# Kernel tuning notes

Measured on AMD Instinct MI355X. Metric: run time of the kernel, lower is better.

The kernel has to match this reference:

```python
import jax, jax.numpy as jnp
import numpy as np

N_NODES = 100000
N_EDGES = 1600000
FEAT = 128
HID = 128
CLASSES = 10
GRAPHS = 64


def gcn_conv(x, W, b, src, dst, n):
    # PyG GCNConv: h = x @ W; add self-loops; symmetric deg^{-1/2} norm; scatter-add; + bias
    h = x @ W
    src_f = jnp.concatenate([src, jnp.arange(n, dtype=src.dtype)])
    dst_f = jnp.concatenate([dst, jnp.arange(n, dtype=dst.dtype)])
    deg = jax.ops.segment_sum(jnp.ones_like(dst_f, dtype=h.dtype), dst_f, num_segments=n)
    dinv = jax.lax.rsqrt(jnp.where(deg > 0, deg, 1.0))
    norm = dinv[src_f] * dinv[dst_f]              # [E+N]
    msg = h[src_f] * norm[:, None]                # gather + scale
    out = jax.ops.segment_sum(msg, dst_f, num_segments=n)  # scatter-add
    return out + b


def global_mean_pool(x, batch, num_graphs):
    s = jax.ops.segment_sum(x, batch, num_segments=num_graphs)
    cnt = jax.ops.segment_sum(jnp.ones_like(batch, dtype=x.dtype), batch, num_segments=num_graphs)
    return s / jnp.maximum(cnt, 1.0)[:, None]


def setup_inputs() -> dict:
    key = jax.random.key(0)
    ks = jax.random.split(key, 10)
    x = jax.random.normal(ks[0], (N_NODES, FEAT), dtype=jnp.float32)
    edge_index = jax.random.randint(ks[1], (2, N_EDGES), 0, N_NODES, dtype=jnp.int64)
    batch = jnp.sort(jax.random.randint(ks[2], (N_NODES,), 0, GRAPHS, dtype=jnp.int64))
    def glorot(k, fi, fo):
        s = float(np.sqrt(6.0 / (fi + fo)))
        return jax.random.uniform(k, (fi, fo), jnp.float32, -s, s)
    return {
        "x": x, "edge_index": edge_index, "batch": batch,
        "W1": glorot(ks[3], FEAT, HID), "b1": jnp.zeros((HID,), jnp.float32),
        "W2": glorot(ks[4], HID, HID), "b2": jnp.zeros((HID,), jnp.float32),
        "W3": glorot(ks[5], HID, HID), "b3": jnp.zeros((HID,), jnp.float32),
        "Wlin": glorot(ks[6], HID, CLASSES), "blin": jnp.zeros((CLASSES,), jnp.float32),
    }


def reference(x, edge_index, batch, W1, b1, W2, b2, W3, b3, Wlin, blin):
    src, dst = edge_index[0], edge_index[1]
    n = x.shape[0]
    h = jax.nn.relu(gcn_conv(x, W1, b1, src, dst, n))
    h = jax.nn.relu(gcn_conv(h, W2, b2, src, dst, n))
    h = gcn_conv(h, W3, b3, src, dst, n)
    emb = global_mean_pool(h, batch, GRAPHS)      # [GRAPHS, HID]
    # dropout(p=0.5) is identity in eval mode
    logits = emb @ Wlin + blin                    # [GRAPHS, CLASSES]
    return logits, jnp.squeeze(emb)
```

## Files before the change

### kernel.cpp

```cpp
#include <hip/hip_runtime.h>
#include <hip/hip_bf16.h>
#include <stdint.h>

typedef unsigned int uint32;
typedef __attribute__((ext_vector_type(8))) short short8;
typedef __attribute__((ext_vector_type(4))) float float4v;
typedef __attribute__((ext_vector_type(2))) float f32x2;

#define FEAT 128
#define NGRAPH 64
#define GB   256
#define NBK  512
#define QPG  8

__device__ __forceinline__ float bf2f_lo(uint32 v) {
    union { uint32 i; float f; } u; u.i = v << 16; return u.f;
}
__device__ __forceinline__ float bf2f_hi(uint32 v) {
    union { uint32 i; float f; } u; u.i = v & 0xffff0000u; return u.f;
}
__device__ __forceinline__ unsigned short f2bf(float f) {
    uint32 u = __builtin_bit_cast(uint32, f);
    uint32 r = (u + 0x7fffu + ((u >> 16) & 1u)) >> 16;
    return (unsigned short)r;
}
__device__ __forceinline__ uint32 f2bf2(float lo, float hi) {
    return (uint32)f2bf(lo) | ((uint32)f2bf(hi) << 16);
}

__global__ void k_bhist(const int* __restrict__ dst, int* __restrict__ bhistT,
                        const float* __restrict__ W1, const float* __restrict__ W2,
                        const float* __restrict__ W3, unsigned short* __restrict__ o1,
                        unsigned short* __restrict__ o2, unsigned short* __restrict__ o3,
                        int E) {
    int t = threadIdx.x, blk = blockIdx.x;
    if (blk >= GB) {
        int b2 = blk - GB;
        int wid = b2 >> 3;
        const float* W = (wid == 0) ? W1 : (wid == 1) ? W2 : W3;
        unsigned short* out = (wid == 0) ? o1 : (wid == 1) ? o2 : o3;
        int e = (b2 & 7) * 256 + t;
        int kt = e >> 9, ct = (e >> 6) & 7, lane = e & 63;
        int krow = kt * 32 + (lane >> 4) * 8;
        int col = ct * 16 + (lane & 15);
#pragma unroll
        for (int j = 0; j < 8; j++)
            out[e * 8 + j] = f2bf(W[(krow + j) * FEAT + col]);
        return;
    }
    __shared__ int h[NBK];
    for (int b = t; b < NBK; b += 256) h[b] = 0;
    __syncthreads();
    int chunk = (E + GB - 1) / GB;
    int lo = blk * chunk, hi = min(lo + chunk, E);
    for (int e = lo + t; e < hi; e += 256)
        atomicAdd(&h[dst[e] >> 8], 1);
    __syncthreads();
    for (int b = t; b < NBK; b += 256) bhistT[b * GB + blk] = h[b];
}

__global__ void k_boffs_a(int* __restrict__ bhistT, int* __restrict__ btot) {
    int b = blockIdx.x, l = threadIdx.x;
    int v[4];
    int base = b * GB + l * 4;
#pragma unroll
    for (int j = 0; j < 4; j++) v[j] = bhistT[base + j];
    int s = v[0] + v[1] + v[2] + v[3];
    int incl = s;
    for (int off = 1; off < 64; off <<= 1) {
        int u = __shfl_up(incl, off);
        if (l >= off) incl += u;
    }
    int excl = incl - s;
    int p0 = excl, p1 = p0 + v[0], p2 = p1 + v[1], p3 = p2 + v[2];
    bhistT[base + 0] = p0; bhistT[base + 1] = p1;
    bhistT[base + 2] = p2; bhistT[base + 3] = p3;
    if (l == 63) btot[b] = incl;
}

__global__ void k_bscat(const int* __restrict__ src, const int* __restrict__ dst,
                        const int* __restrict__ bhistT, const int* __restrict__ btot,
                        uint32* __restrict__ ebuf, int E) {
    __shared__ int cur[NBK];
    int t = threadIdx.x, blk = blockIdx.x;
    int o0 = btot[t], o1 = btot[t + 256];
    cur[t] = o0; cur[t + 256] = o1;
    __syncthreads();
    for (int off = 1; off < NBK; off <<= 1) {
        int v0 = (t >= off) ? cur[t - off] : 0;
        int v1 = (t + 256 >= off) ? cur[t + 256 - off] : 0;
        __syncthreads();
        cur[t] += v0; cur[t + 256] += v1;
        __syncthreads();
    }
    cur[t]       = cur[t]       - o0 + bhistT[t * GB + blk];
    cur[t + 256] = cur[t + 256] - o1 + bhistT[(t + 256) * GB + blk];
    __syncthreads();
    int chunk = (E + GB - 1) / GB;
    int lo = blk * chunk, hi = min(lo + chunk, E);
    for (int e = lo + t; e < hi; e += 256) {
        int d = dst[e], s = src[e];
        int b = d >> 8;
        int p = atomicAdd(&cur[b], 1);
        ebuf[p] = ((uint32)s << 8) | (uint32)(d & 255);
    }
}

__global__ void k_csr(const uint32* __restrict__ ebuf, const int* __restrict__ btot,
                      float* __restrict__ dinv, int* __restrict__ rowp,
                      int* __restrict__ csrc, int N, int E) {
    __shared__ int h[256];
    __shared__ int cur[256];
    __shared__ int ebase;
    int t = threadIdx.x, b = blockIdx.x;
    int part = 0;
    for (int j = t; j < b; j += 256) part += btot[j];
    cur[t] = part;
    __syncthreads();
    for (int off = 128; off > 0; off >>= 1) {
        if (t < off) cur[t] += cur[t + off];
        __syncthreads();
    }
    if (t == 0) ebase = cur[0];
    __syncthreads();
    int e0 = ebase, e1 = e0 + btot[b];
    h[t] = 0;
    __syncthreads();
    for (int e = e0 + t; e < e1; e += 256)
        atomicAdd(&h[ebuf[e] & 255u], 1);
    __syncthreads();
    int deg = h[t];
    cur[t] = deg;
    __syncthreads();
    for (int off = 1; off < 256; off <<= 1) {
        int v = (t >= off) ? cur[t - off] : 0;
        __syncthreads();
        cur[t] += v;
        __syncthreads();
    }
    int r = e0 + cur[t] - deg;
    int node = b * 256 + t;
    if (node < N) {
        rowp[node] = r;
        dinv[node] = rsqrtf((float)deg + 1.0f);
    }
    if (b == 0 && t == 0) rowp[N] = E;
    cur[t] = r;
    __syncthreads();
    for (int e = e0 + t; e < e1; e += 256) {
        uint32 v = ebuf[e];
        int p = atomicAdd(&cur[v & 255u], 1);
        csrc[p] = (int)(v >> 8);
    }
}

template <bool F32IN>
__global__ void k_gemm(const void* __restrict__ Xp,
                       const unsigned short* __restrict__ Wswz,
                       const float* __restrict__ dinv,
                       unsigned short* __restrict__ Hb, int N, int ntiles) {
    __shared__ unsigned short Wl[FEAT * FEAT];
    {
        const uint4* Wg = (const uint4*)Wswz;
        uint4* Ws = (uint4*)Wl;
        for (int i = threadIdx.x; i < 2048; i += 256) Ws[i] = Wg[i];
    }
    __syncthreads();

    int wave = threadIdx.x >> 6, lane = threadIdx.x & 63;
    int m = lane & 15, q = lane >> 4;
    const short8* Bl = (const short8*)Wl;

    for (int tb = blockIdx.x; tb < ntiles; tb += gridDim.x) {
        int r0 = (tb * 4 + wave) * 16;
        if (r0 >= N) continue;

        int arow = r0 + m; if (arow >= N) arow = N - 1;
        short8 a[4];
        if (F32IN) {
            const float* Ar = (const float*)Xp + (long)arow * FEAT;
#pragma unroll
            for (int kt = 0; kt < 4; kt++) {
                float4 u = *(const float4*)(Ar + kt * 32 + q * 8);
                float4 v = *(const float4*)(Ar + kt * 32 + q * 8 + 4);
                short8 tv;
                tv[0] = (short)f2bf(u.x); tv[1] = (short)f2bf(u.y);
                tv[2] = (short)f2bf(u.z); tv[3] = (short)f2bf(u.w);
                tv[4] = (short)f2bf(v.x); tv[5] = (short)f2bf(v.y);
                tv[6] = (short)f2bf(v.z); tv[7] = (short)f2bf(v.w);
                a[kt] = tv;
            }
        } else {
            const short8* Ar = (const short8*)((const unsigned short*)Xp + (long)arow * FEAT);
#pragma unroll
            for (int kt = 0; kt < 4; kt++) a[kt] = Ar[kt * 4 + q];
        }

        float4v acc[8];
#pragma unroll
        for (int ct = 0; ct < 8; ct++) acc[ct] = (float4v){0.f, 0.f, 0.f, 0.f};
#pragma unroll
        for (int ct = 0; ct < 8; ct++) {
            acc[ct] = __builtin_amdgcn_mfma_f32_16x16x32_bf16(Bl[(0 * 8 + ct) * 64 + lane], a[0], acc[ct], 0, 0, 0);
            acc[ct] = __builtin_amdgcn_mfma_f32_16x16x32_bf16(Bl[(1 * 8 + ct) * 64 + lane], a[1], acc[ct], 0, 0, 0);
            acc[ct] = __builtin_amdgcn_mfma_f32_16x16x32_bf16(Bl[(2 * 8 + ct) * 64 + lane], a[2], acc[ct], 0, 0, 0);
            acc[ct] = __builtin_amdgcn_mfma_f32_16x16x32_bf16(Bl[(3 * 8 + ct) * 64 + lane], a[3], acc[ct], 0, 0, 0);
        }

        int node = r0 + m;
        bool ok = (node < N);
        float d = ok ? dinv[node] : 0.f;
#pragma unroll
        for (int ct = 0; ct < 8; ct++) {
            if (ok) {
                uint2 o;
                o.x = f2bf2(acc[ct][0] * d, acc[ct][1] * d);
                o.y = f2bf2(acc[ct][2] * d, acc[ct][3] * d);
                ((uint2*)(Hb + (long)node * FEAT + ct * 16))[q] = o;
            }
        }
    }
}

template <int RELU>
__global__ void k_agg(const uint32* __restrict__ Hb,
                      const int* __restrict__ rowp, const int* __restrict__ csrc,
                      const float* __restrict__ dinv, const float* __restrict__ bias,
                      uint32* __restrict__ OUTb, int N) {
    int wave = threadIdx.x >> 6, lane = threadIdx.x & 63;
    int i = blockIdx.x * 4 + wave;
    if (i >= N) return;
    int f = lane & 15, quarter = lane >> 4;
    const uint4* H4 = (const uint4*)Hb;
    f32x2 c0 = {0.f, 0.f}, c1 = c0, c2 = c0, c3 = c0;
    int e0 = rowp[i], e1 = rowp[i + 1];
    int e = e0;
    for (; e + 16 <= e1; e += 16) {
        int  s[4];
        uint4 h[4];
#pragma unroll
        for (int j = 0; j < 4; j++) s[j] = csrc[e + 4 * j + quarter];
#pragma unroll
        for (int j = 0; j < 4; j++) h[j] = H4[(long)s[j] * 16 + f];
#pragma unroll
        for (int j = 0; j < 4; j++) {
            f32x2 u;
            u.x = bf2f_lo(h[j].x); u.y = bf2f_hi(h[j].x); c0 += u;
            u.x = bf2f_lo(h[j].y); u.y = bf2f_hi(h[j].y); c1 += u;
            u.x = bf2f_lo(h[j].z); u.y = bf2f_hi(h[j].z); c2 += u;
            u.x = bf2f_lo(h[j].w); u.y = bf2f_hi(h[j].w); c3 += u;
        }
    }
    {
        int r = e1 - e;
        int  s[4];
        uint4 h[4];
#pragma unroll
        for (int j = 0; j < 4; j++) {
            int idx = 4 * j + quarter;
            if (idx < r) s[j] = csrc[e + idx];
        }
#pragma unroll
        for (int j = 0; j < 4; j++)
            if (4 * j + quarter < r) h[j] = H4[(long)s[j] * 16 + f];
#pragma unroll
        for (int j = 0; j < 4; j++)
            if (4 * j + quarter < r) {
                f32x2 u;
                u.x = bf2f_lo(h[j].x); u.y = bf2f_hi(h[j].x); c0 += u;
                u.x = bf2f_lo(h[j].y); u.y = bf2f_hi(h[j].y); c1 += u;
                u.x = bf2f_lo(h[j].z); u.y = bf2f_hi(h[j].z); c2 += u;
                u.x = bf2f_lo(h[j].w); u.y = bf2f_hi(h[j].w); c3 += u;
            }
    }
    c0.x += __shfl_xor(c0.x, 16); c0.y += __shfl_xor(c0.y, 16);
    c1.x += __shfl_xor(c1.x, 16); c1.y += __shfl_xor(c1.y, 16);
    c2.x += __shfl_xor(c2.x, 16); c2.y += __shfl_xor(c2.y, 16);
    c3.x += __shfl_xor(c3.x, 16); c3.y += __shfl_xor(c3.y, 16);
    c0.x += __shfl_xor(c0.x, 32); c0.y += __shfl_xor(c0.y, 32);
    c1.x += __shfl_xor(c1.x, 32); c1.y += __shfl_xor(c1.y, 32);
    c2.x += __shfl_xor(c2.x, 32); c2.y += __shfl_xor(c2.y, 32);
    c3.x += __shfl_xor(c3.x, 32); c3.y += __shfl_xor(c3.y, 32);
    if (quarter == 0) {
        uint4 hv = H4[(long)i * 16 + f];
        c0.x += bf2f_lo(hv.x); c0.y += bf2f_hi(hv.x);
        c1.x += bf2f_lo(hv.y); c1.y += bf2f_hi(hv.y);
        c2.x += bf2f_lo(hv.z); c2.y += bf2f_hi(hv.z);
        c3.x += bf2f_lo(hv.w); c3.y += bf2f_hi(hv.w);
        float di = dinv[i];
        const float4* b4 = (const float4*)bias;
        float4 bb0 = b4[2 * f], bb1 = b4[2 * f + 1];
        c0.x = c0.x * di + bb0.x; c0.y = c0.y * di + bb0.y;
        c1.x = c1.x * di + bb0.z; c1.y = c1.y * di + bb0.w;
        c2.x = c2.x * di + bb1.x; c2.y = c2.y * di + bb1.y;
        c3.x = c3.x * di + bb1.z; c3.y = c3.y * di + bb1.w;
        if (RELU) {
            c0.x = fmaxf(c0.x, 0.f); c0.y = fmaxf(c0.y, 0.f);
            c1.x = fmaxf(c1.x, 0.f); c1.y = fmaxf(c1.y, 0.f);
            c2.x = fmaxf(c2.x, 0.f); c2.y = fmaxf(c2.y, 0.f);
            c3.x = fmaxf(c3.x, 0.f); c3.y = fmaxf(c3.y, 0.f);
        }
        uint4 o;
        o.x = f2bf2(c0.x, c0.y);
        o.y = f2bf2(c1.x, c1.y);
        o.z = f2bf2(c2.x, c2.y);
        o.w = f2bf2(c3.x, c3.y);
        ((uint4*)OUTb)[(long)i * 16 + f] = o;
    }
}

__global__ void k_pool2(const uint32* __restrict__ Gb, const int* __restrict__ batch,
                        float* __restrict__ pool, int N) {
    __shared__ float spx[256], spy[256];
    int t = threadIdx.x;
    int g = blockIdx.x >> 3, qtr = blockIdx.x & (QPG - 1);
    int lo, hi;
    { int l = 0, h = N; while (l < h) { int m = (l + h) >> 1; if (batch[m] < g) l = m + 1; else h = m; } lo = l; }
    { int l = lo, h = N; while (l < h) { int m = (l + h) >> 1; if (batch[m] < g + 1) l = m + 1; else h = m; } hi = l; }
    int cnt = hi - lo;
    int chunk = (cnt + QPG - 1) / QPG;
    int lo2 = lo + qtr * chunk;
    int hi2 = min(lo2 + chunk, hi);
    int f = t & 63, sub = t >> 6;
    float ax = 0.f, ay = 0.f;
#pragma unroll 4
    for (int i = lo2 + sub; i < hi2; i += 4) {
        uint32 v = Gb[(long)i * 64 + f];
        ax += bf2f_lo(v); ay += bf2f_hi(v);
    }
    spx[t] = ax; spy[t] = ay;
    __syncthreads();
    if (t < 64) {
        float sx = spx[t] + spx[t + 64] + spx[t + 128] + spx[t + 192];
        float sy = spy[t] + spy[t + 64] + spy[t + 128] + spy[t + 192];
        float* pr = pool + ((size_t)qtr * NGRAPH + g) * FEAT;
        pr[2 * t]     = sx;
        pr[2 * t + 1] = sy;
    }
}

__global__ void k_final(const float* __restrict__ pool, const int* __restrict__ batch,
                        const float* __restrict__ Wlin, const float* __restrict__ blin,
                        float* __restrict__ out, int N) {
    __shared__ float es[FEAT];
    __shared__ int lohi[2];
    int g = blockIdx.x, t = threadIdx.x;
    if (t < 2) {
        int key = g + t;
        int lo = 0, hi = N;
        while (lo < hi) {
            int mid = (lo + hi) >> 1;
            if (batch[mid] < key) lo = mid + 1; else hi = mid;
        }
        lohi[t] = lo;
    }
    float s = 0.f;
#pragma unroll
    for (int r = 0; r < QPG; r++) s += pool[(r * NGRAPH + g) * FEAT + t];
    __syncthreads();
    float c = (float)max(lohi[1] - lohi[0], 1);
    float e = s / c;
    es[t] = e;
    out[NGRAPH * 10 + g * FEAT + t] = e;
    __syncthreads();
    if (t < 10) {
        float a = blin[t];
        for (int k = 0; k < FEAT; k++)
            a += es[k] * Wlin[k * 10 + t];
        out[g * 10 + t] = a;
    }
}

extern "C" void kernel_launch(void* const* d_in, const int* in_sizes, int n_in,
                              void* d_out, int out_size, void* d_ws, size_t ws_size,
                              hipStream_t stream) {
    const float* x    = (const float*)d_in[0];
    const int*   ei   = (const int*)d_in[1];
    const int*   batch= (const int*)d_in[2];
    const float* W1   = (const float*)d_in[3];
    const float* b1   = (const float*)d_in[4];
    const float* W2   = (const float*)d_in[5];
    const float* b2   = (const float*)d_in[6];
    const float* W3   = (const float*)d_in[7];
    const float* b3   = (const float*)d_in[8];
    const float* Wlin = (const float*)d_in[9];
    const float* blin = (const float*)d_in[10];

    const int N = in_sizes[2];
    const int E = in_sizes[1] / 2;
    const int* src = ei;
    const int* dst = ei + E;
    const int NB = (N + 255) >> 8;

    char* w = (char*)d_ws;
    auto take = [&](size_t bytes) {
        char* p = w;
        w += (bytes + 255) & ~(size_t)255;
        return p;
    };
    float*  dinv   = (float*) take((size_t)N * 4);
    int*    rowp   = (int*)   take((size_t)(N + 1) * 4);
    int*    csrc   = (int*)   take((size_t)E * 4);
    uint32* ebuf   = (uint32*)take((size_t)E * 4);
    int*    bhistT = (int*)   take((size_t)GB * NBK * 4);
    int*    btot   = (int*)   take((size_t)NBK * 4);
    uint32* hbuf   = (uint32*)take((size_t)N * FEAT * 2);
    uint32* gbuf   = (uint32*)take((size_t)N * FEAT * 2);
    unsigned short* w1s = (unsigned short*)take(FEAT * FEAT * 2);
    unsigned short* w2s = (unsigned short*)take(FEAT * FEAT * 2);
    unsigned short* w3s = (unsigned short*)take(FEAT * FEAT * 2);
    float*  pool   = (float*) take((size_t)QPG * NGRAPH * FEAT * 4);
    (void)ws_size; (void)n_in; (void)out_size;

    k_bhist  <<<GB + 24, 256, 0, stream>>>(dst, bhistT,
                                           W1, W2, W3, w1s, w2s, w3s, E);
    k_boffs_a<<<NBK, 64, 0, stream>>>(bhistT, btot);
    k_bscat  <<<GB, 256, 0, stream>>>(src, dst, bhistT, btot, ebuf, E);
    k_csr    <<<NB, 256, 0, stream>>>(ebuf, btot, dinv, rowp, csrc, N, E);

    const int tile_blocks = (N + 63) / 64;
    const int agg_blocks  = (N + 3) / 4;
    const int gemm_grid   = (tile_blocks < 512) ? tile_blocks : 512;

    k_gemm<true> <<<gemm_grid, 256, 0, stream>>>(x, w1s, dinv, (unsigned short*)hbuf, N, tile_blocks);
    k_agg<1><<<agg_blocks, 256, 0, stream>>>(hbuf, rowp, csrc, dinv, b1, gbuf, N);
    k_gemm<false><<<gemm_grid, 256, 0, stream>>>(gbuf, w2s, dinv, (unsigned short*)hbuf, N, tile_blocks);
    k_agg<1><<<agg_blocks, 256, 0, stream>>>(hbuf, rowp, csrc, dinv, b2, gbuf, N);
    k_gemm<false><<<gemm_grid, 256, 0, stream>>>(gbuf, w3s, dinv, (unsigned short*)hbuf, N, tile_blocks);
    k_agg<0><<<agg_blocks, 256, 0, stream>>>(hbuf, rowp, csrc, dinv, b3, gbuf, N);

    k_pool2<<<NGRAPH * QPG, 256, 0, stream>>>(gbuf, batch, pool, N);
    k_final<<<NGRAPH, 128, 0, stream>>>(pool, batch, Wlin, blin, (float*)d_out, N);
}
```

Measured before the change: 398.7 us.

## Fuse neighbor aggregation with next-layer GEMM via LDS staging per wave

Adds a k_fused kernel in which each wave gathers and aggregates 16 nodes one after another, applies bias and ReLU, stages the bf16 rows in LDS, and then multiplies them by the next layer's weight with MFMA. Layers 1 and 2 therefore no longer write the aggregated features to global memory and read them back. k_gemm also drops its persistent grid-stride loop and launches one tile per block. The cost is that the gather, which is latency bound, now runs 16 nodes serially per wave. The weight and staging buffers also take a lot of LDS per block, which may lower occupancy and latency hiding compared with the one-wave-per-node aggregation kernel.

```diff
diff --git a/kernel.cpp b/kernel.cpp
--- a/kernel.cpp
+++ b/kernel.cpp
@@ -158,7 +158,7 @@
 __global__ void k_gemm(const void* __restrict__ Xp,
                        const unsigned short* __restrict__ Wswz,
                        const float* __restrict__ dinv,
-                       unsigned short* __restrict__ Hb, int N, int ntiles) {
+                       unsigned short* __restrict__ Hb, int N) {
     __shared__ unsigned short Wl[FEAT * FEAT];
     {
         const uint4* Wg = (const uint4*)Wswz;
@@ -168,56 +168,53 @@
     __syncthreads();
 
     int wave = threadIdx.x >> 6, lane = threadIdx.x & 63;
+    int r0 = (blockIdx.x * 4 + wave) * 16;
+    if (r0 >= N) return;
     int m = lane & 15, q = lane >> 4;
+
+    int arow = r0 + m; if (arow >= N) arow = N - 1;
+    short8 a[4];
+    if (F32IN) {
+        const float* Ar = (const float*)Xp + (long)arow * FEAT;
+#pragma unroll
+        for (int kt = 0; kt < 4; kt++) {
+            float4 u = *(const float4*)(Ar + kt * 32 + q * 8);
+            float4 v = *(const float4*)(Ar + kt * 32 + q * 8 + 4);
+            short8 tv;
+            tv[0] = (short)f2bf(u.x); tv[1] = (short)f2bf(u.y);
+            tv[2] = (short)f2bf(u.z); tv[3] = (short)f2bf(u.w);
+            tv[4] = (short)f2bf(v.x); tv[5] = (short)f2bf(v.y);
+            tv[6] = (short)f2bf(v.z); tv[7] = (short)f2bf(v.w);
+            a[kt] = tv;
+        }
+    } else {
+        const short8* Ar = (const short8*)((const unsigned short*)Xp + (long)arow * FEAT);
+#pragma unroll
+        for (int kt = 0; kt < 4; kt++) a[kt] = Ar[kt * 4 + q];
+    }
+
     const short8* Bl = (const short8*)Wl;
-
-    for (int tb = blockIdx.x; tb < ntiles; tb += gridDim.x) {
-        int r0 = (tb * 4 + wave) * 16;
-        if (r0 >= N) continue;
-
-        int arow = r0 + m; if (arow >= N) arow = N - 1;
-        short8 a[4];
-        if (F32IN) {
-            const float* Ar = (const float*)Xp + (long)arow * FEAT;
-#pragma unroll
-            for (int kt = 0; kt < 4; kt++) {
-                float4 u = *(const float4*)(Ar + kt * 32 + q * 8);
-                float4 v = *(const float4*)(Ar + kt * 32 + q * 8 + 4);
-                short8 tv;
-                tv[0] = (short)f2bf(u.x); tv[1] = (short)f2bf(u.y);
-                tv[2] = (short)f2bf(u.z); tv[3] = (short)f2bf(u.w);
-                tv[4] = (short)f2bf(v.x); tv[5] = (short)f2bf(v.y);
-                tv[6] = (short)f2bf(v.z); tv[7] = (short)f2bf(v.w);
-                a[kt] = tv;
-            }
-        } else {
-            const short8* Ar = (const short8*)((const unsigned short*)Xp + (long)arow * FEAT);
-#pragma unroll
-            for (int kt = 0; kt < 4; kt++) a[kt] = Ar[kt * 4 + q];
-        }
-
-        float4v acc[8];
-#pragma unroll
-        for (int ct = 0; ct < 8; ct++) acc[ct] = (float4v){0.f, 0.f, 0.f, 0.f};
-#pragma unroll
-        for (int ct = 0; ct < 8; ct++) {
-            acc[ct] = __builtin_amdgcn_mfma_f32_16x16x32_bf16(Bl[(0 * 8 + ct) * 64 + lane], a[0], acc[ct], 0, 0, 0);
-            acc[ct] = __builtin_amdgcn_mfma_f32_16x16x32_bf16(Bl[(1 * 8 + ct) * 64 + lane], a[1], acc[ct], 0, 0, 0);
-            acc[ct] = __builtin_amdgcn_mfma_f32_16x16x32_bf16(Bl[(2 * 8 + ct) * 64 + lane], a[2], acc[ct], 0, 0, 0);
-            acc[ct] = __builtin_amdgcn_mfma_f32_16x16x32_bf16(Bl[(3 * 8 + ct) * 64 + lane], a[3], acc[ct], 0, 0, 0);
-        }
-
-        int node = r0 + m;
-        bool ok = (node < N);
-        float d = ok ? dinv[node] : 0.f;
-#pragma unroll
-        for (int ct = 0; ct < 8; ct++) {
-            if (ok) {
-                uint2 o;
-                o.x = f2bf2(acc[ct][0] * d, acc[ct][1] * d);
-                o.y = f2bf2(acc[ct][2] * d, acc[ct][3] * d);
-                ((uint2*)(Hb + (long)node * FEAT + ct * 16))[q] = o;
-            }
+    float4v acc[8];
+#pragma unroll
+    for (int ct = 0; ct < 8; ct++) acc[ct] = (float4v){0.f, 0.f, 0.f, 0.f};
+#pragma unroll
+    for (int ct = 0; ct < 8; ct++) {
+        acc[ct] = __builtin_amdgcn_mfma_f32_16x16x32_bf16(Bl[(0 * 8 + ct) * 64 + lane], a[0], acc[ct], 0, 0, 0);
+        acc[ct] = __builtin_amdgcn_mfma_f32_16x16x32_bf16(Bl[(1 * 8 + ct) * 64 + lane], a[1], acc[ct], 0, 0, 0);
+        acc[ct] = __builtin_amdgcn_mfma_f32_16x16x32_bf16(Bl[(2 * 8 + ct) * 64 + lane], a[2], acc[ct], 0, 0, 0);
+        acc[ct] = __builtin_amdgcn_mfma_f32_16x16x32_bf16(Bl[(3 * 8 + ct) * 64 + lane], a[3], acc[ct], 0, 0, 0);
+    }
+
+    int node = r0 + m;
+    bool ok = (node < N);
+    float d = ok ? dinv[node] : 0.f;
+#pragma unroll
+    for (int ct = 0; ct < 8; ct++) {
+        if (ok) {
+            uint2 o;
+            o.x = f2bf2(acc[ct][0] * d, acc[ct][1] * d);
+            o.y = f2bf2(acc[ct][2] * d, acc[ct][3] * d);
+            ((uint2*)(Hb + (long)node * FEAT + ct * 16))[q] = o;
         }
     }
 }
@@ -309,6 +306,132 @@
     }
 }
 
+__global__ void k_fused(const uint32* __restrict__ Hin,
+                        const int* __restrict__ rowp, const int* __restrict__ csrc,
+                        const float* __restrict__ dinv, const float* __restrict__ bias,
+                        const unsigned short* __restrict__ Wswz,
+                        unsigned short* __restrict__ Hout, int N) {
+    __shared__ unsigned short Wl[FEAT * FEAT];
+    __shared__ uint4 stage[4][16 * 17];
+    {
+        const uint4* Wg = (const uint4*)Wswz;
+        uint4* Ws = (uint4*)Wl;
+        for (int i = threadIdx.x; i < 2048; i += 256) Ws[i] = Wg[i];
+    }
+    __syncthreads();
+
+    int wave = threadIdx.x >> 6, lane = threadIdx.x & 63;
+    int f = lane & 15, quarter = lane >> 4;
+    int r0 = (blockIdx.x * 4 + wave) * 16;
+    const uint4* H4 = (const uint4*)Hin;
+
+    for (int m = 0; m < 16; m++) {
+        int i = r0 + m;
+        uint4 o = {0u, 0u, 0u, 0u};
+        if (i < N) {
+            f32x2 c0 = {0.f, 0.f}, c1 = c0, c2 = c0, c3 = c0;
+            int e0 = rowp[i], e1 = rowp[i + 1];
+            int e = e0;
+            for (; e + 16 <= e1; e += 16) {
+                int  s[4];
+                uint4 h[4];
+#pragma unroll
+                for (int j = 0; j < 4; j++) s[j] = csrc[e + 4 * j + quarter];
+#pragma unroll
+                for (int j = 0; j < 4; j++) h[j] = H4[(long)s[j] * 16 + f];
+#pragma unroll
+                for (int j = 0; j < 4; j++) {
+                    f32x2 u;
+                    u.x = bf2f_lo(h[j].x); u.y = bf2f_hi(h[j].x); c0 += u;
+                    u.x = bf2f_lo(h[j].y); u.y = bf2f_hi(h[j].y); c1 += u;
+                    u.x = bf2f_lo(h[j].z); u.y = bf2f_hi(h[j].z); c2 += u;
+                    u.x = bf2f_lo(h[j].w); u.y = bf2f_hi(h[j].w); c3 += u;
+                }
+            }
+            {
+                int r = e1 - e;
+                int  s[4];
+                uint4 h[4];
+#pragma unroll
+                for (int j = 0; j < 4; j++) {
+                    int idx = 4 * j + quarter;
+                    if (idx < r) s[j] = csrc[e + idx];
+                }
+#pragma unroll
+                for (int j = 0; j < 4; j++)
+                    if (4 * j + quarter < r) h[j] = H4[(long)s[j] * 16 + f];
+#pragma unroll
+                for (int j = 0; j < 4; j++)
+                    if (4 * j + quarter < r) {
+                        f32x2 u;
+                        u.x = bf2f_lo(h[j].x); u.y = bf2f_hi(h[j].x); c0 += u;
+                        u.x = bf2f_lo(h[j].y); u.y = bf2f_hi(h[j].y); c1 += u;
+                        u.x = bf2f_lo(h[j].z); u.y = bf2f_hi(h[j].z); c2 += u;
+                        u.x = bf2f_lo(h[j].w); u.y = bf2f_hi(h[j].w); c3 += u;
+                    }
+            }
+            c0.x += __shfl_xor(c0.x, 16); c0.y += __shfl_xor(c0.y, 16);
+            c1.x += __shfl_xor(c1.x, 16); c1.y += __shfl_xor(c1.y, 16);
+            c2.x += __shfl_xor(c2.x, 16); c2.y += __shfl_xor(c2.y, 16);
+            c3.x += __shfl_xor(c3.x, 16); c3.y += __shfl_xor(c3.y, 16);
+            c0.x += __shfl_xor(c0.x, 32); c0.y += __shfl_xor(c0.y, 32);
+            c1.x += __shfl_xor(c1.x, 32); c1.y += __shfl_xor(c1.y, 32);
+            c2.x += __shfl_xor(c2.x, 32); c2.y += __shfl_xor(c2.y, 32);
+            c3.x += __shfl_xor(c3.x, 32); c3.y += __shfl_xor(c3.y, 32);
+            if (quarter == 0) {
+                uint4 hv = H4[(long)i * 16 + f];
+                c0.x += bf2f_lo(hv.x); c0.y += bf2f_hi(hv.x);
+                c1.x += bf2f_lo(hv.y); c1.y += bf2f_hi(hv.y);
+                c2.x += bf2f_lo(hv.z); c2.y += bf2f_hi(hv.z);
+                c3.x += bf2f_lo(hv.w); c3.y += bf2f_hi(hv.w);
+                float di = dinv[i];
+                const float4* b4 = (const float4*)bias;
+                float4 bb0 = b4[2 * f], bb1 = b4[2 * f + 1];
+                c0.x = fmaxf(c0.x * di + bb0.x, 0.f); c0.y = fmaxf(c0.y * di + bb0.y, 0.f);
+                c1.x = fmaxf(c1.x * di + bb0.z, 0.f); c1.y = fmaxf(c1.y * di + bb0.w, 0.f);
+                c2.x = fmaxf(c2.x * di + bb1.x, 0.f); c2.y = fmaxf(c2.y * di + bb1.y, 0.f);
+                c3.x = fmaxf(c3.x * di + bb1.z, 0.f); c3.y = fmaxf(c3.y * di + bb1.w, 0.f);
+                o.x = f2bf2(c0.x, c0.y);
+                o.y = f2bf2(c1.x, c1.y);
+                o.z = f2bf2(c2.x, c2.y);
+                o.w = f2bf2(c3.x, c3.y);
+            }
+        }
+        if (quarter == 0) stage[wave][m * 17 + f] = o;
+    }
+
+    int q = quarter;
+    short8 a[4];
+#pragma unroll
+    for (int kt = 0; kt < 4; kt++)
+        a[kt] = *(const short8*)&stage[wave][f * 17 + kt * 4 + q];
+
+    const short8* Bl = (const short8*)Wl;
+    float4v acc[8];
+#pragma unroll
+    for (int ct = 0; ct < 8; ct++) acc[ct] = (float4v){0.f, 0.f, 0.f, 0.f};
+#pragma unroll
+    for (int ct = 0; ct < 8; ct++) {
+        acc[ct] = __builtin_amdgcn_mfma_f32_16x16x32_bf16(Bl[(0 * 8 + ct) * 64 + lane], a[0], acc[ct], 0, 0, 0);
+        acc[ct] = __builtin_amdgcn_mfma_f32_16x16x32_bf16(Bl[(1 * 8 + ct) * 64 + lane], a[1], acc[ct], 0, 0, 0);
+        acc[ct] = __builtin_amdgcn_mfma_f32_16x16x32_bf16(Bl[(2 * 8 + ct) * 64 + lane], a[2], acc[ct], 0, 0, 0);
+        acc[ct] = __builtin_amdgcn_mfma_f32_16x16x32_bf16(Bl[(3 * 8 + ct) * 64 + lane], a[3], acc[ct], 0, 0, 0);
+    }
+
+    int node = r0 + f;
+    bool ok = (node < N);
+    float d = ok ? dinv[node] : 0.f;
+#pragma unroll
+    for (int ct = 0; ct < 8; ct++) {
+        if (ok) {
+            uint2 o2;
+            o2.x = f2bf2(acc[ct][0] * d, acc[ct][1] * d);
+            o2.y = f2bf2(acc[ct][2] * d, acc[ct][3] * d);
+            ((uint2*)(Hout + (long)node * FEAT + ct * 16))[q] = o2;
+        }
+    }
+}
+
 __global__ void k_pool2(const uint32* __restrict__ Gb, const int* __restrict__ batch,
                         float* __restrict__ pool, int N) {
     __shared__ float spx[256], spy[256];
@@ -419,15 +542,13 @@
     k_csr    <<<NB, 256, 0, stream>>>(ebuf, btot, dinv, rowp, csrc, N, E);
 
     const int tile_blocks = (N + 63) / 64;
-    const int agg_blocks  = (N + 3) / 4;
-    const int gemm_grid   = (tile_blocks < 512) ? tile_blocks : 512;
-
-    k_gemm<true> <<<gemm_grid, 256, 0, stream>>>(x, w1s, dinv, (unsigned short*)hbuf, N, tile_blocks);
-    k_agg<1><<<agg_blocks, 256, 0, stream>>>(hbuf, rowp, csrc, dinv, b1, gbuf, N);
-    k_gemm<false><<<gemm_grid, 256, 0, stream>>>(gbuf, w2s, dinv, (unsigned short*)hbuf, N, tile_blocks);
-    k_agg<1><<<agg_blocks, 256, 0, stream>>>(hbuf, rowp, csrc, dinv, b2, gbuf, N);
-    k_gemm<false><<<gemm_grid, 256, 0, stream>>>(gbuf, w3s, dinv, (unsigned short*)hbuf, N, tile_blocks);
-    k_agg<0><<<agg_blocks, 256, 0, stream>>>(hbuf, rowp, csrc, dinv, b3, gbuf, N);
+
+    k_gemm<true><<<tile_blocks, 256, 0, stream>>>(x, w1s, dinv, (unsigned short*)hbuf, N);
+    k_fused<<<tile_blocks, 256, 0, stream>>>(hbuf, rowp, csrc, dinv, b1, w2s,
+                                             (unsigned short*)gbuf, N);
+    k_fused<<<tile_blocks, 256, 0, stream>>>(gbuf, rowp, csrc, dinv, b2, w3s,
+                                             (unsigned short*)hbuf, N);
+    k_agg<0><<<(N + 3) / 4, 256, 0, stream>>>(hbuf, rowp, csrc, dinv, b3, gbuf, N);
 
     k_pool2<<<NGRAPH * QPG, 256, 0, stream>>>(gbuf, batch, pool, N);
     k_final<<<NGRAPH, 128, 0, stream>>>(pool, batch, Wlin, blin, (float*)d_out, N);
```

New measurement: 498.7 us. +25.1%, slower.
